# Performance work log

Measured on AMD Instinct MI355X. Metric: run time of the kernel, lower is better.

## Reference

```python
import jax, jax.numpy as jnp
import numpy as np

HEADS = 20


def cape_embed(f, P):
    # f: [b, s, d], P: [b, s, 4, 4]; rotate channel groups of 4 by P
    b, s, d = f.shape
    f4 = f.reshape(b, s, d // 4, 4)
    out = jnp.einsum('bsik,bskj->bsij', f4, P)
    return out.reshape(b, s, d)


def setup_inputs() -> dict:
    key = jax.random.key(0)
    ks = jax.random.split(key, 9)
    bt, l, d = 2, 1024, 1280  # (b*t_out, tokens, channels)
    t_out, b = 2, 1
    sd = 1.0 / np.sqrt(d)
    return {
        'hidden_states': jax.random.normal(ks[0], (bt, l, d), jnp.float32),
        'p_out': jax.random.normal(ks[1], (b, t_out, 4, 4), jnp.float32) * 0.5,
        'p_out_inv': jax.random.normal(ks[2], (b, t_out, 4, 4), jnp.float32) * 0.5,
        'Wq': jax.random.normal(ks[3], (d, d), jnp.float32) * sd,
        'Wk': jax.random.normal(ks[4], (d, d), jnp.float32) * sd,
        'Wv': jax.random.normal(ks[5], (d, d), jnp.float32) * sd,
        'Wo': jax.random.normal(ks[6], (d, d), jnp.float32) * sd,
        'bo': jnp.zeros((d,), jnp.float32),
    }


def reference(hidden_states, p_out, p_out_inv, Wq, Wk, Wv, Wo, bo):
    residual = hidden_states  # [(b t_out), l, d]
    b = p_out.shape[0]
    t_out = p_out.shape[1]
    bt, l, d = hidden_states.shape
    s = t_out * l
    hd = d // HEADS
    scale = hd ** -0.5

    # rearrange '(b t_out) l d -> b (t_out l) d'
    hs = hidden_states.reshape(b, s, d)

    q = hs @ Wq
    k = hs @ Wk
    v = hs @ Wv

    # repeat per-frame CAPE matrices over spatial tokens: 'b t f g -> b (t l) f g'
    Pq = jnp.repeat(p_out_inv, l, axis=1)  # [b, s, 4, 4]
    Pk = jnp.repeat(p_out, l, axis=1)      # self-attn: p_in := p_out
    q = cape_embed(q, Pq)
    k = cape_embed(k, Pk)

    # head split: [b, s, d] -> [b, h, s, hd]
    qh = q.reshape(b, s, HEADS, hd).transpose(0, 2, 1, 3)
    kh = k.reshape(b, s, HEADS, hd).transpose(0, 2, 1, 3)
    vh = v.reshape(b, s, HEADS, hd).transpose(0, 2, 1, 3)

    scores = jnp.einsum('bhsd,bhtd->bhst', qh, kh) * scale
    probs = jax.nn.softmax(scores, axis=-1)
    out = jnp.einsum('bhst,bhtd->bhsd', probs, vh)

    out = out.transpose(0, 2, 1, 3).reshape(b, s, d)
    out = out @ Wo + bo

    # rearrange 'b (t_out l) d -> (b t_out) l d'
    out = out.reshape(bt, l, d)
    out = out + residual  # residual_connection; rescale_output_factor = 1.0
    return out
```

## Files before the change

### kernel.cpp

```cpp
#include <hip/hip_runtime.h>

typedef short short8 __attribute__((ext_vector_type(8)));
typedef short short4v __attribute__((ext_vector_type(4)));
typedef float f32x4 __attribute__((ext_vector_type(4)));
typedef float float4v __attribute__((ext_vector_type(4)));
typedef __bf16 bf16x8 __attribute__((ext_vector_type(8)));
typedef _Float16 half4 __attribute__((ext_vector_type(4)));
typedef _Float16 half2v __attribute__((ext_vector_type(2)));

__device__ __forceinline__ short f2bf(float x) {
  unsigned u = __builtin_bit_cast(unsigned, x);
  u += 0x7fffu + ((u >> 16) & 1u);
  return (short)(u >> 16);
}

__device__ __forceinline__ f32x4 mfma16(short8 a, short8 b, f32x4 c) {
  return __builtin_amdgcn_mfma_f32_16x16x32_bf16(
      __builtin_bit_cast(bf16x8, a), __builtin_bit_cast(bf16x8, b), c, 0, 0, 0);
}

__device__ __forceinline__ void async16(void* lds, const void* g) {
  __builtin_amdgcn_global_load_lds(
      (const __attribute__((address_space(1))) unsigned*)g,
      (__attribute__((address_space(3))) unsigned*)lds, 16, 0, 0);
}

__global__ __launch_bounds__(256) void capeT_all_kernel(
    const float* __restrict__ Wq, const float* __restrict__ Wk,
    const float* __restrict__ Wv, const float* __restrict__ Wo,
    const float* __restrict__ p_inv, const float* __restrict__ p_out,
    float qscale, short* __restrict__ BT0, short* __restrict__ BT1,
    short* __restrict__ wo_t, const float* __restrict__ hs,
    short* __restrict__ hs_bf) {
  const int ND = 1280, KD = 1280;
  const size_t SEC = (size_t)1280 * 1280;
  int z = blockIdx.z;
  int tx = threadIdx.x, ty = threadIdx.y;
  if (z == 4) {
    int t = ty * 32 + tx;
    int base = ((blockIdx.y * 40 + blockIdx.x) * 256 + t) * 2;
    const int n4 = 2048 * 1280 / 4;
#pragma unroll
    for (int r = 0; r < 2; r++) {
      int i = base + r;
      if (i < n4) {
        float4v v = *(const float4v*)(hs + (size_t)i * 4);
        short4v o;
#pragma unroll
        for (int j = 0; j < 4; j++) o[j] = f2bf(v[j]);
        *(short4v*)(hs_bf + (size_t)i * 4) = o;
      }
    }
    return;
  }
  const float* W;
  const float* P;
  float scale = 1.0f;
  short *d0, *d1;
  if (z == 0) { W = Wq; P = p_inv; scale = qscale; d0 = BT0; d1 = BT1; }
  else if (z == 1) { W = Wk; P = p_out; d0 = BT0 + SEC; d1 = BT1 + SEC; }
  else if (z == 2) { W = Wv; P = nullptr; d0 = BT0 + 2 * SEC; d1 = BT1 + 2 * SEC; }
  else { W = Wo; P = nullptr; d0 = wo_t; d1 = nullptr; }

  __shared__ float tile[32][33];
  int bn = blockIdx.x * 32, bk = blockIdx.y * 32;
  for (int i = ty; i < 32; i += 8)
    tile[i][tx] = W[(size_t)(bk + i) * ND + bn + tx];
  __syncthreads();
  for (int c = ty; c < 32; c += 8) {
    float v0, v1;
    if (P) {
      int g = c & ~3, jj = c & 3;
      float a0 = 0.f, a1 = 0.f;
#pragma unroll
      for (int j = 0; j < 4; j++) {
        float wv = tile[tx][g + j];
        a0 += wv * P[j * 4 + jj];
        a1 += wv * P[16 + j * 4 + jj];
      }
      v0 = a0 * scale;
      v1 = a1 * scale;
    } else {
      v0 = v1 = tile[tx][c] * scale;
    }
    size_t o = (size_t)(bn + c) * KD + bk + tx;
    d0[o] = f2bf(v0);
    if (d1) d1[o] = f2bf(v1);
  }
}


__global__ __launch_bounds__(256) void gemm128_qkv_kernel(
    const short* __restrict__ A, const short* __restrict__ B0,
    const short* __restrict__ B1, int M, int N, int K,
    short* __restrict__ qb, short* __restrict__ ktl,
    _Float16* __restrict__ vtl) {
  __shared__ __align__(16) short As[2][128][32];
  __shared__ __align__(16) short Bs[2][128][32];
  int tid = threadIdx.x;
  int l = tid & 63, w = tid >> 6;
  int wr = w >> 1, wc = w & 1;
  int lr = l & 15, lg = l >> 4;
  int bm = blockIdx.y * 128, bn = blockIdx.x * 128;
  const short* BT = (bm >= 1024) ? B1 : B0;
  f32x4 acc[4][4] = {};

  auto stage = [&](int b, int k0) {
    const short* ga = A + (size_t)(bm + (tid >> 2)) * K + k0 + (tid & 3) * 8;
    const short* gb = BT + (size_t)(bn + (tid >> 2)) * K + k0 + (tid & 3) * 8;
    char* la = (char*)&As[b][0][0] + w * 1024;
    char* lb = (char*)&Bs[b][0][0] + w * 1024;
    async16(la, ga);
    async16(la + 4096, ga + (size_t)64 * K);
    async16(lb, gb);
    async16(lb + 4096, gb + (size_t)64 * K);
  };

  auto compute = [&](int b) {
    const short* Ab = &As[b][0][0];
    const short* Bb = &Bs[b][0][0];
    short8 af[4], bf_[4];
#pragma unroll
    for (int mi = 0; mi < 4; mi++)
      af[mi] = *(const short8*)(Ab + (wr * 64 + mi * 16 + lr) * 32 + lg * 8);
#pragma unroll
    for (int nj = 0; nj < 4; nj++)
      bf_[nj] = *(const short8*)(Bb + (wc * 64 + nj * 16 + lr) * 32 + lg * 8);
#pragma unroll
    for (int mi = 0; mi < 4; mi++)
#pragma unroll
      for (int nj = 0; nj < 4; nj++)
        acc[mi][nj] = mfma16(af[mi], bf_[nj], acc[mi][nj]);
  };

  int nk = K >> 5;
  stage(0, 0);
  for (int ks = 0; ks < nk; ks += 2) {
    __syncthreads();
    if (ks + 1 < nk) stage(1, (ks + 1) << 5);
    compute(0);
    __syncthreads();
    if (ks + 2 < nk) stage(0, (ks + 2) << 5);
    compute(1);
  }

#pragma unroll
  for (int mi = 0; mi < 4; mi++)
#pragma unroll
    for (int nj = 0; nj < 4; nj++)
#pragma unroll
      for (int i = 0; i < 4; i++) {
        int row = bm + wr * 64 + mi * 16 + lg * 4 + i;
        int col = bn + wc * 64 + nj * 16 + lr;
        float v = acc[mi][nj][i];
        int s = row;
        if (col < 1280) {
          qb[(((size_t)(col >> 6)) * 2048 + s) * 64 + (col & 63)] = f2bf(v);
        } else if (col < 2560) {
          int cc = col - 1280;
          int h = cc >> 6, d = cc & 63;
          int kt = s >> 6, r = s & 63;
          int kcol = (((d >> 3) ^ (r & 7)) << 3) | (d & 7);
          ktl[(((size_t)h * 32 + kt) * 64 + r) * 64 + kcol] = f2bf(v);
        } else {
          int cc = col - 2560;
          int h = cc >> 6, dv = cc & 63;
          int kt = s >> 6, kk = s & 63;
          int vcol = (((kk >> 2) ^ (dv & 15)) << 2) | (kk & 3);
          vtl[(((size_t)h * 32 + kt) * 64 + dv) * 64 + vcol] = (_Float16)v;
        }
      }
}


__global__ __launch_bounds__(256) void gemm64_o_kernel(
    const short* __restrict__ A, const short* __restrict__ BT,
    int M, int N, int K, const float* __restrict__ bias,
    const float* __restrict__ resid, float* __restrict__ out) {
  __shared__ __align__(16) short As[2][64][32];
  __shared__ __align__(16) short Bs[2][64][32];
  int tid = threadIdx.x;
  int l = tid & 63, w = tid >> 6;
  int wr = w >> 1, wc = w & 1;
  int lr = l & 15, lg = l >> 4;
  int bm = blockIdx.y * 64, bn = blockIdx.x * 64;
  f32x4 acc[2][2] = {};

  auto stage = [&](int b, int k0) {
    const short* ga = A + (size_t)(bm + (tid >> 2)) * K + k0 + (tid & 3) * 8;
    const short* gb = BT + (size_t)(bn + (tid >> 2)) * K + k0 + (tid & 3) * 8;
    async16((char*)&As[b][0][0] + w * 1024, ga);
    async16((char*)&Bs[b][0][0] + w * 1024, gb);
  };

  auto compute = [&](int b) {
    const short* Ab = &As[b][0][0];
    const short* Bb = &Bs[b][0][0];
    short8 af[2], bf_[2];
#pragma unroll
    for (int mi = 0; mi < 2; mi++)
      af[mi] = *(const short8*)(Ab + (wr * 32 + mi * 16 + lr) * 32 + lg * 8);
#pragma unroll
    for (int nj = 0; nj < 2; nj++)
      bf_[nj] = *(const short8*)(Bb + (wc * 32 + nj * 16 + lr) * 32 + lg * 8);
#pragma unroll
    for (int mi = 0; mi < 2; mi++)
#pragma unroll
      for (int nj = 0; nj < 2; nj++)
        acc[mi][nj] = mfma16(af[mi], bf_[nj], acc[mi][nj]);
  };

  int nk = K >> 5;
  stage(0, 0);
  for (int ks = 0; ks < nk; ks += 2) {
    __syncthreads();
    if (ks + 1 < nk) stage(1, (ks + 1) << 5);
    compute(0);
    __syncthreads();
    if (ks + 2 < nk) stage(0, (ks + 2) << 5);
    compute(1);
  }

#pragma unroll
  for (int mi = 0; mi < 2; mi++)
#pragma unroll
    for (int nj = 0; nj < 2; nj++)
#pragma unroll
      for (int i = 0; i < 4; i++) {
        int row = bm + wr * 32 + mi * 16 + lg * 4 + i;
        int col = bn + wc * 32 + nj * 16 + lr;
        out[(size_t)row * N + col] =
            acc[mi][nj][i] + bias[col] + resid[(size_t)row * N + col];
      }
}

__global__ __launch_bounds__(256) void attn_kernel(
    const short* __restrict__ qb, const short* __restrict__ k_tiled,
    const _Float16* __restrict__ v_tiled, short* __restrict__ attn_out) {
  const int S = 2048, HD = 64;
  int h = blockIdx.x;
  int qblk = blockIdx.y;
  int tid = threadIdx.x;
  int w = tid >> 6, l = tid & 63;
  int lr = l & 15, lg = l >> 4;
  int q0 = qblk * 64 + w * 16;

  __shared__ __align__(16) short Kl[3][64][64];
  __shared__ __align__(16) _Float16 Vl[3][64][64];

  const short* qptr = qb + ((size_t)h * S + q0 + lr) * HD;
  short8 qf0 = *(const short8*)(qptr + lg * 8);
  short8 qf1 = *(const short8*)(qptr + 32 + lg * 8);

  auto stageKV = [&](int b, int kt) {
    const short* gk = k_tiled + (((size_t)h * 32 + kt) << 12) + tid * 8;
    const _Float16* gv = v_tiled + (((size_t)h * 32 + kt) << 12) + tid * 8;
    char* lk = (char*)&Kl[b][0][0] + w * 1024;
    char* lv = (char*)&Vl[b][0][0] + w * 1024;
    async16(lk, gk);
    async16(lk + 4096, gk + 2048);
    async16(lv, gv);
    async16(lv + 4096, gv + 2048);
  };

  float m = -1e30f, lsum = 0.f;
  f32x4 oacc[4] = {};

  auto compute_tile = [&](int buf) {
    const short* Kb = &Kl[buf][0][0];
    const _Float16* Vb = &Vl[buf][0][0];
    f32x4 st[4];
    __builtin_amdgcn_s_setprio(1);
#pragma unroll
    for (int kk = 0; kk < 4; kk++) {
      int r = kk * 16 + lr;
      int sw = r & 7;
      short8 kf0 = *(const short8*)(Kb + r * 64 + ((lg ^ sw) << 3));
      short8 kf1 = *(const short8*)(Kb + r * 64 + (((4 + lg) ^ sw) << 3));
      f32x4 s0 = {};
      s0 = mfma16(kf0, qf0, s0);
      s0 = mfma16(kf1, qf1, s0);
      st[kk] = s0;
    }
    __builtin_amdgcn_s_setprio(0);
    float m0 = fmaxf(fmaxf(st[0][0], st[0][1]), fmaxf(st[0][2], st[0][3]));
    float m1 = fmaxf(fmaxf(st[1][0], st[1][1]), fmaxf(st[1][2], st[1][3]));
    float m2 = fmaxf(fmaxf(st[2][0], st[2][1]), fmaxf(st[2][2], st[2][3]));
    float m3 = fmaxf(fmaxf(st[3][0], st[3][1]), fmaxf(st[3][2], st[3][3]));
    float pmax = fmaxf(fmaxf(m0, m1), fmaxf(m2, m3));
    if (!__all(pmax <= m + 8.0f)) {
      float tm = pmax;
      tm = fmaxf(tm, __shfl_xor(tm, 16));
      tm = fmaxf(tm, __shfl_xor(tm, 32));
      float mnew = fmaxf(m, tm);
      float fac = __builtin_amdgcn_exp2f(m - mnew);
      lsum *= fac;
#pragma unroll
      for (int i = 0; i < 4; i++) {
        float fi = __shfl(fac, lg * 4 + i);
#pragma unroll
        for (int nb = 0; nb < 4; nb++) oacc[nb][i] *= fi;
      }
      m = mnew;
    }
    half4 pf[4];
    float ps[4];
#pragma unroll
    for (int kk = 0; kk < 4; kk++) {
      float p0 = __builtin_amdgcn_exp2f(st[kk][0] - m);
      float p1 = __builtin_amdgcn_exp2f(st[kk][1] - m);
      float p2 = __builtin_amdgcn_exp2f(st[kk][2] - m);
      float p3 = __builtin_amdgcn_exp2f(st[kk][3] - m);
      half2v lo = __builtin_bit_cast(half2v, __builtin_amdgcn_cvt_pkrtz(p0, p1));
      half2v hi = __builtin_bit_cast(half2v, __builtin_amdgcn_cvt_pkrtz(p2, p3));
      pf[kk][0] = lo[0]; pf[kk][1] = lo[1];
      pf[kk][2] = hi[0]; pf[kk][3] = hi[1];
      ps[kk] = (p0 + p1) + (p2 + p3);
    }
    lsum += (ps[0] + ps[1]) + (ps[2] + ps[3]);
#pragma unroll
    for (int kk = 0; kk < 4; kk++) {
      half4 vf[4];
#pragma unroll
      for (int nb = 0; nb < 4; nb++) {
        int dv = nb * 16 + lr;
        vf[nb] = *(const half4*)(Vb + dv * 64 + ((((kk << 2) + lg) ^ lr) << 2));
      }
      __builtin_amdgcn_s_setprio(1);
#pragma unroll
      for (int nb = 0; nb < 4; nb++)
        oacc[nb] = __builtin_amdgcn_mfma_f32_16x16x16f16(pf[kk], vf[nb], oacc[nb], 0, 0, 0);
      __builtin_amdgcn_s_setprio(0);
    }
  };

  stageKV(0, 0);
  stageKV(1, 1);
  for (int t = 0; t < 32; ++t) {
    if (t < 31) {
      asm volatile("s_waitcnt vmcnt(4)" ::: "memory");
    } else {
      asm volatile("s_waitcnt vmcnt(0)" ::: "memory");
    }
    __builtin_amdgcn_sched_barrier(0);
    __builtin_amdgcn_s_barrier();
    __builtin_amdgcn_sched_barrier(0);
    if (t + 2 < 32) stageKV((t + 2) % 3, t + 2);
    compute_tile(t % 3);
  }

  lsum += __shfl_xor(lsum, 16);
  lsum += __shfl_xor(lsum, 32);

#pragma unroll
  for (int i = 0; i < 4; i++) {
    float li = __shfl(lsum, lg * 4 + i);
    float inv = 1.0f / li;
    int row = q0 + lg * 4 + i;
#pragma unroll
    for (int nb = 0; nb < 4; nb++)
      attn_out[(size_t)row * 1280 + h * 64 + nb * 16 + lr] = f2bf(oacc[nb][i] * inv);
  }
}


extern "C" void kernel_launch(void* const* d_in, const int* in_sizes, int n_in,
                              void* d_out, int out_size, void* d_ws, size_t ws_size,
                              hipStream_t stream) {
  const float* hs = (const float*)d_in[0];
  const float* p_out = (const float*)d_in[1];
  const float* p_inv = (const float*)d_in[2];
  const float* Wq = (const float*)d_in[3];
  const float* Wk = (const float*)d_in[4];
  const float* Wv = (const float*)d_in[5];
  const float* Wo = (const float*)d_in[6];
  const float* bo = (const float*)d_in[7];
  float* out = (float*)d_out;
  char* ws = (char*)d_ws;

  short* hs_bf = (short*)(ws + 0);
  short* BT0 = (short*)(ws + 5242880);
  short* BT1 = (short*)(ws + 15073280);
  short* wo_t = (short*)(ws + 24903680);
  short* q_bf = (short*)(ws + 28180480);
  short* k_tiled = (short*)(ws + 33423360);
  _Float16* v_tiled = (_Float16*)(ws + 38666240);
  short* attn_bf = (short*)(ws + 43909120);

  const float QSCALE = 0.125f * 1.44269504f;

  capeT_all_kernel<<<dim3(40, 40, 5), dim3(32, 8), 0, stream>>>(
      Wq, Wk, Wv, Wo, p_inv, p_out, QSCALE, BT0, BT1, wo_t, hs, hs_bf);

  gemm128_qkv_kernel<<<dim3(30, 16), 256, 0, stream>>>(
      hs_bf, BT0, BT1, 2048, 3840, 1280, q_bf, k_tiled, v_tiled);

  attn_kernel<<<dim3(20, 32), 256, 0, stream>>>(q_bf, k_tiled, v_tiled, attn_bf);

  gemm64_o_kernel<<<dim3(20, 32), 256, 0, stream>>>(
      attn_bf, wo_t, 2048, 1280, 1280, bo, hs, out);
}
```

Baseline: 121.5 us.

## Split attention over two KV halves and merge partials in a combine kernel

The attention kernel now gets a third grid dimension that splits the 32 KV tiles into two halves of 16. Each half writes unnormalized fp32 partial outputs plus per-row max and sum into workspace. A new combine kernel rescales and merges the two partials, then writes the bf16 attention output. The goal is to double the block count for better CU occupancy and load balance. In exchange it adds a round trip of fp32 partials through global memory and an extra launch, and it replaces the 3-buffer vmcnt-gated pipeline with a simpler 2-buffer __syncthreads scheme.

```diff
diff --git a/kernel.cpp b/kernel.cpp
--- a/kernel.cpp
+++ b/kernel.cpp
@@ -236,17 +236,20 @@
 
 __global__ __launch_bounds__(256) void attn_kernel(
     const short* __restrict__ qb, const short* __restrict__ k_tiled,
-    const _Float16* __restrict__ v_tiled, short* __restrict__ attn_out) {
+    const _Float16* __restrict__ v_tiled, float* __restrict__ opart,
+    float2* __restrict__ ml) {
   const int S = 2048, HD = 64;
   int h = blockIdx.x;
   int qblk = blockIdx.y;
+  int half = blockIdx.z;
+  int kt_base = half * 16;
   int tid = threadIdx.x;
   int w = tid >> 6, l = tid & 63;
   int lr = l & 15, lg = l >> 4;
   int q0 = qblk * 64 + w * 16;
 
-  __shared__ __align__(16) short Kl[3][64][64];
-  __shared__ __align__(16) _Float16 Vl[3][64][64];
+  __shared__ __align__(16) short Kl[2][64][64];
+  __shared__ __align__(16) _Float16 Vl[2][64][64];
 
   const short* qptr = qb + ((size_t)h * S + q0 + lr) * HD;
   short8 qf0 = *(const short8*)(qptr + lg * 8);
@@ -334,32 +337,62 @@
     }
   };
 
-  stageKV(0, 0);
-  stageKV(1, 1);
-  for (int t = 0; t < 32; ++t) {
-    if (t < 31) {
-      asm volatile("s_waitcnt vmcnt(4)" ::: "memory");
-    } else {
-      asm volatile("s_waitcnt vmcnt(0)" ::: "memory");
-    }
-    __builtin_amdgcn_sched_barrier(0);
-    __builtin_amdgcn_s_barrier();
-    __builtin_amdgcn_sched_barrier(0);
-    if (t + 2 < 32) stageKV((t + 2) % 3, t + 2);
-    compute_tile(t % 3);
+  stageKV(0, kt_base);
+  for (int t2 = 0; t2 < 16; t2 += 2) {
+    __syncthreads();
+    if (t2 + 1 < 16) stageKV(1, kt_base + t2 + 1);
+    compute_tile(0);
+    __syncthreads();
+    if (t2 + 2 < 16) stageKV(0, kt_base + t2 + 2);
+    compute_tile(1);
   }
 
   lsum += __shfl_xor(lsum, 16);
   lsum += __shfl_xor(lsum, 32);
 
+  size_t blk = (size_t)half * 640 + h * 32 + qblk;
+  float* obase = opart + blk * 4096;
 #pragma unroll
   for (int i = 0; i < 4; i++) {
-    float li = __shfl(lsum, lg * 4 + i);
-    float inv = 1.0f / li;
-    int row = q0 + lg * 4 + i;
+    int ql = w * 16 + lg * 4 + i;
 #pragma unroll
     for (int nb = 0; nb < 4; nb++)
-      attn_out[(size_t)row * 1280 + h * 64 + nb * 16 + lr] = f2bf(oacc[nb][i] * inv);
+      obase[ql * 64 + nb * 16 + lr] = oacc[nb][i];
+  }
+  if (lg == 0) {
+    float2 v;
+    v.x = m;
+    v.y = lsum;
+    ml[blk * 64 + w * 16 + lr] = v;
+  }
+}
+
+__global__ __launch_bounds__(256) void attn_combine_kernel(
+    const float* __restrict__ opart, const float2* __restrict__ ml,
+    short* __restrict__ attn_out) {
+  int h = blockIdx.x, qb = blockIdx.y;
+  int t = threadIdx.x;
+  int ql = t >> 2, dq = (t & 3) * 16;
+  size_t blk = (size_t)h * 32 + qb;
+  float2 ml0 = ml[blk * 64 + ql];
+  float2 ml1 = ml[(size_t)640 * 64 + blk * 64 + ql];
+  float M = fmaxf(ml0.x, ml1.x);
+  float a0 = __builtin_amdgcn_exp2f(ml0.x - M);
+  float a1 = __builtin_amdgcn_exp2f(ml1.x - M);
+  float inv = 1.0f / (ml0.y * a0 + ml1.y * a1);
+  float s0 = a0 * inv, s1 = a1 * inv;
+  const float* o0 = opart + blk * 4096 + ql * 64 + dq;
+  const float* o1 = o0 + (size_t)640 * 4096;
+  int row = qb * 64 + ql;
+  short* dst = attn_out + (size_t)row * 1280 + h * 64 + dq;
+#pragma unroll
+  for (int d = 0; d < 16; d += 4) {
+    float4v v0 = *(const float4v*)(o0 + d);
+    float4v v1 = *(const float4v*)(o1 + d);
+    short4v o;
+#pragma unroll
+    for (int j = 0; j < 4; j++) o[j] = f2bf(v0[j] * s0 + v1[j] * s1);
+    *(short4v*)(dst + d) = o;
   }
 }
 
@@ -386,6 +419,8 @@
   short* k_tiled = (short*)(ws + 33423360);
   _Float16* v_tiled = (_Float16*)(ws + 38666240);
   short* attn_bf = (short*)(ws + 43909120);
+  float* opart = (float*)(ws + 0);
+  float2* ml = (float2*)(ws + 22020096);
 
   const float QSCALE = 0.125f * 1.44269504f;
 
@@ -395,7 +430,10 @@
   gemm128_qkv_kernel<<<dim3(30, 16), 256, 0, stream>>>(
       hs_bf, BT0, BT1, 2048, 3840, 1280, q_bf, k_tiled, v_tiled);
 
-  attn_kernel<<<dim3(20, 32), 256, 0, stream>>>(q_bf, k_tiled, v_tiled, attn_bf);
+  attn_kernel<<<dim3(20, 32, 2), 256, 0, stream>>>(
+      q_bf, k_tiled, v_tiled, opart, ml);
+
+  attn_combine_kernel<<<dim3(20, 32), 256, 0, stream>>>(opart, ml, attn_bf);
 
   gemm64_o_kernel<<<dim3(20, 32), 256, 0, stream>>>(
       attn_bf, wo_t, 2048, 1280, 1280, bo, hs, out);
```

New measurement: 125.1 us. +3.0%, slower.
